# Kernel tuning notes

Hardware: AMD Instinct MI355X
Metric: run time of the kernel (lower is better)

Reference implementation:

```python
import jax, jax.numpy as jnp
import numpy as np

N = 100000
E = 3200000
F_IN = 256
F_OUT = 256
HID = 64


def setup_inputs() -> dict:
    key = jax.random.key(0)
    ks = jax.random.split(key, 16)
    stdv = 1.0 / np.sqrt(F_OUT)
    std_att = 1.0 / np.sqrt(HID)
    std_att_vec = 1.0 / np.sqrt(3.0)
    u = lambda k, shape, s: jax.random.uniform(k, shape, jnp.float32, -s, s)
    return {
        "inputx": jax.random.normal(ks[0], (N, F_IN), jnp.float32),
        "row_A": jax.random.randint(ks[1], (E,), 0, N),
        "col_A": jax.random.randint(ks[2], (E,), 0, N),
        "val_A": jax.random.uniform(ks[3], (E,), jnp.float32),
        "row_A2": jax.random.randint(ks[4], (E,), 0, N),
        "col_A2": jax.random.randint(ks[5], (E,), 0, N),
        "val_A2": jax.random.uniform(ks[6], (E,), jnp.float32),
        "weight_A": u(ks[7], (F_IN, F_OUT), stdv),
        "weight_A2": u(ks[8], (F_IN, F_OUT), stdv),
        "weight_mlp": u(ks[9], (F_IN, F_OUT), stdv),
        "W_k0": u(ks[10], (F_OUT, HID), std_att),
        "W_k1": u(ks[11], (F_OUT, HID), std_att),
        "W_k2": u(ks[12], (F_OUT, HID), std_att),
        "att_vec_A": u(ks[13], (F_OUT, HID), std_att),
        "att_vec_A2": u(ks[14], (F_OUT, HID), std_att),
        "att_vec_mlp": u(ks[15], (F_OUT, HID), std_att),
        "att_vec": u(jax.random.fold_in(key, 99), (3, 3), std_att_vec),
    }


def _spmm(row, col, val, x, n):
    # COO sparse-dense matmul: out[r] += val_e * x[c]
    return jax.ops.segment_sum(val[:, None] * x[col], row, num_segments=n)


def reference(inputx, row_A, col_A, val_A, row_A2, col_A2, val_A2,
              weight_A, weight_A2, weight_mlp, W_k0, W_k1, W_k2,
              att_vec_A, att_vec_A2, att_vec_mlp, att_vec):
    n = inputx.shape[0]
    out_A = jax.nn.relu(_spmm(row_A, col_A, val_A, inputx @ weight_A, n))
    out_A2 = jax.nn.relu(_spmm(row_A2, col_A2, val_A2, inputx @ weight_A2, n))
    out_mlp = jax.nn.relu(inputx @ weight_mlp)
    # attention gating
    T = 3.0
    k0 = jnp.mean(out_A @ W_k0, axis=0, keepdims=True)    # [1, HID]
    k1 = jnp.mean(out_A2 @ W_k1, axis=0, keepdims=True)
    k2 = jnp.mean(out_mlp @ W_k2, axis=0, keepdims=True)
    logits = jnp.concatenate([
        (out_A @ att_vec_A) @ k0.T,      # [N, 1]
        (out_A2 @ att_vec_A2) @ k1.T,
        (out_mlp @ att_vec_mlp) @ k2.T,
    ], axis=1)                           # [N, 3]
    att = jax.nn.softmax((jax.nn.sigmoid(logits) @ att_vec) / T, axis=1)
    return 3.0 * (att[:, 0:1] * out_A + att[:, 1:2] * out_A2 + att[:, 2:3] * out_mlp)
```

## Files before the change

kernel.cpp:

```cpp
#include <hip/hip_runtime.h>

typedef __bf16 bf16;
typedef __bf16 bf16x4 __attribute__((ext_vector_type(4)));
typedef __bf16 bf16x8 __attribute__((ext_vector_type(8)));
typedef float f32x4 __attribute__((ext_vector_type(4)));

__device__ __forceinline__ f32x4 bf2f(bf16x4 v){
  f32x4 r; r[0]=(float)v[0]; r[1]=(float)v[1]; r[2]=(float)v[2]; r[3]=(float)v[3]; return r;
}

#define NBMAX 1600
#define NBP   1601
#define CHUNK 4096
#define CAP   2560
#define CSRCAP 2816

__global__ __launch_bounds__(256) void k_xcvt(const float* __restrict__ X, bf16* __restrict__ Xb, int total){
  int i = (blockIdx.x*256 + threadIdx.x)*8;
  if (i + 8 <= total){
    float4 a = *(const float4*)(X+i);
    float4 b = *(const float4*)(X+i+4);
    bf16x8 v;
    v[0]=(bf16)a.x; v[1]=(bf16)a.y; v[2]=(bf16)a.z; v[3]=(bf16)a.w;
    v[4]=(bf16)b.x; v[5]=(bf16)b.y; v[6]=(bf16)b.z; v[7]=(bf16)b.w;
    *(bf16x8*)(Xb+i) = v;
  }
}

__global__ __launch_bounds__(256) void k_wt(const float* __restrict__ W0, const float* __restrict__ W1,
                                            const float* __restrict__ W2, bf16* __restrict__ WT3){
  int n = blockIdx.x, mat = blockIdx.y, k = threadIdx.x;
  const float* W = (mat==0)?W0:((mat==1)?W1:W2);
  WT3[mat*65536 + n*256 + k] = (bf16)W[k*256 + n];
}

__global__ __launch_bounds__(512) void k_binT(const int* __restrict__ rowA, const int* __restrict__ colA,
    const float* __restrict__ valA, const int* __restrict__ rowA2, const int* __restrict__ colA2,
    const float* __restrict__ valA2, int* __restrict__ gcur,
    int2* __restrict__ pTA, int2* __restrict__ pTA2, int E, int NB){
  __shared__ int hist[NBMAX];
  int mat = blockIdx.y;
  const int* row = mat? rowA2 : rowA;
  const int* col = mat? colA2 : colA;
  const float* val = mat? valA2 : valA;
  int2* pT = mat? pTA2 : pTA;
  int t = threadIdx.x;
  for (int i=t; i<NB; i+=512) hist[i] = 0;
  __syncthreads();
  int base = blockIdx.x * CHUNK;
  int endi = base + CHUNK; if (endi > E) endi = E;
  for (int i = base + t; i < endi; i += 512) atomicAdd(&hist[row[i] >> 6], 1);
  __syncthreads();
  for (int i=t; i<NB; i+=512){
    int c = hist[i];
    if (c) hist[i] = i*CAP + atomicAdd(&gcur[mat*NB + i], c);
  }
  __syncthreads();
  for (int i = base + t; i < endi; i += 512){
    int r = row[i];
    int pos = atomicAdd(&hist[r >> 6], 1);
    int2 p; p.x = ((r & 63) << 17) | col[i]; p.y = __float_as_int(val[i]);
    pT[pos] = p;
  }
}

__global__ __launch_bounds__(256) void k_bscan(const int* __restrict__ gcur, int* __restrict__ gstart,
    int NB, int E){
  __shared__ int ss[256];
  __shared__ int carry;
  int mat = blockIdx.x;
  int t = threadIdx.x;
  if (t==0) carry = 0;
  __syncthreads();
  for (int base=0; base<NB; base+=256){
    int i = base + t;
    int v = (i < NB) ? gcur[mat*NB + i] : 0;
    ss[t] = v; __syncthreads();
    for (int off=1; off<256; off<<=1){
      int u = (t>=off)? ss[t-off] : 0;
      __syncthreads();
      ss[t] += u;
      __syncthreads();
    }
    int excl = carry + ss[t] - v;
    if (i < NB) gstart[mat*NBP + i] = excl;
    int tot = ss[255];
    __syncthreads();
    if (t==0) carry += tot;
    __syncthreads();
  }
  if (t==0) gstart[mat*NBP + NB] = E;
}

__global__ __launch_bounds__(256) void k_csr(const int2* __restrict__ pTA, const int2* __restrict__ pTA2,
    const int* __restrict__ gcur, const int* __restrict__ gstart,
    int* __restrict__ rsA, int* __restrict__ rsA2,
    int2* __restrict__ permA, int2* __restrict__ permA2, int N, int NB, int E){
  __shared__ int2 raw[CSRCAP];
  __shared__ unsigned short sidx[CSRCAP];
  __shared__ int fill[64];
  __shared__ int rowst_l[64];
  int mat = blockIdx.y;
  const int2* pT = mat? pTA2 : pTA;
  int2* perm = mat? permA2 : permA;
  int* rs = mat? rsA2 : rsA;
  int b = blockIdx.x;
  int t = threadIdx.x;
  int r0 = b*64;
  int src = b*CAP;
  int cnt = gcur[mat*NB + b];
  if (cnt > CSRCAP) cnt = CSRCAP;
  int dst = gstart[mat*NBP + b];
  if (t < 64) fill[t] = 0;
  __syncthreads();
  for (int i = t; i < cnt; i += 256){
    int2 e = pT[src + i];
    raw[i] = e;
    atomicAdd(&fill[e.x >> 17], 1);
  }
  __syncthreads();
  if (t < 64){
    int v = fill[t];
    int x = v;
#pragma unroll
    for (int off=1; off<64; off<<=1){
      int u = __shfl_up(x, off, 64);
      if (t >= off) x += u;
    }
    int st = x - v;
    rowst_l[t] = st;
    if (r0 + t < N) rs[r0 + t] = dst + st;
    fill[t] = 0;
  }
  __syncthreads();
  for (int i = t; i < cnt; i += 256){
    int rl = raw[i].x >> 17;
    int pos = atomicAdd(&fill[rl], 1);
    sidx[rowst_l[rl] + pos] = (unsigned short)i;
  }
  __syncthreads();
  for (int j = t; j < cnt; j += 256){
    int2 e = raw[sidx[j]];
    int2 o; o.x = e.x & 0x1FFFF; o.y = e.y;
    perm[dst + j] = o;
  }
  if (t == 0 && b == NB-1) rs[N] = E;
}

__global__ __launch_bounds__(256) void k_spmm(const bf16* __restrict__ Xb,
    const int* __restrict__ rsA, const int* __restrict__ rsA2,
    const int2* __restrict__ permA, const int2* __restrict__ permA2,
    bf16* __restrict__ AXb, bf16* __restrict__ A2Xb, int N){
  int mat = blockIdx.y;
  const int* rs = mat? rsA2 : rsA;
  const int2* perm = mat? permA2 : permA;
  bf16* dst = mat? A2Xb : AXb;
  int t = threadIdx.x, lane = t & 63, wv = t >> 6;
  int c = lane*4;
  int rstep = gridDim.x*4;

  for (int row = blockIdx.x*4 + wv; row < N; row += rstep){
    int e = rs[row], eend = rs[row+1];
    f32x4 acc; acc[0]=0.f; acc[1]=0.f; acc[2]=0.f; acc[3]=0.f;

    int2 p0, p1, p2, p3;
    bool have = (e + 3 < eend);
    if (have){ p0 = perm[e]; p1 = perm[e+1]; p2 = perm[e+2]; p3 = perm[e+3]; }
    while (have){
      bf16x4 g0 = *(const bf16x4*)(Xb + (size_t)p0.x*256 + c);
      bf16x4 g1 = *(const bf16x4*)(Xb + (size_t)p1.x*256 + c);
      bf16x4 g2 = *(const bf16x4*)(Xb + (size_t)p2.x*256 + c);
      bf16x4 g3 = *(const bf16x4*)(Xb + (size_t)p3.x*256 + c);
      float v0 = __int_as_float(p0.y), v1 = __int_as_float(p1.y);
      float v2 = __int_as_float(p2.y), v3 = __int_as_float(p3.y);
      e += 4;
      have = (e + 3 < eend);
      if (have){ p0 = perm[e]; p1 = perm[e+1]; p2 = perm[e+2]; p3 = perm[e+3]; }
      acc += v0 * bf2f(g0);
      acc += v1 * bf2f(g1);
      acc += v2 * bf2f(g2);
      acc += v3 * bf2f(g3);
    }
    for (; e < eend; ++e){
      int2 p = perm[e];
      acc += __int_as_float(p.y) * bf2f(*(const bf16x4*)(Xb + (size_t)p.x*256 + c));
    }
    bf16x4 o;
#pragma unroll
    for (int k=0;k<4;k++) o[k] = (bf16)acc[k];
    *(bf16x4*)(dst + (size_t)row*256 + c) = o;
  }
}

__global__ __launch_bounds__(512) void k_gemm(bf16* __restrict__ M0, bf16* __restrict__ M1,
        bf16* __restrict__ M2, const bf16* __restrict__ WT3, float* __restrict__ colsum, int N){
  __shared__ __align__(16) bf16 sA[128*32];
  __shared__ __align__(16) bf16 sB[256*32];
  __shared__ float gcs[256];
  int t = threadIdx.x;
  int lane = t & 63, wave = t>>6, wm = wave>>2, wn = wave&3;
  int mat = blockIdx.y;
  int m0 = blockIdx.x*128;
  const bf16* WT = WT3 + mat*65536;
  bf16* M = (mat==0)?M0:((mat==1)?M1:M2);

  f32x4 acc[4][4];
#pragma unroll
  for (int i=0;i<4;i++)
#pragma unroll
    for (int j=0;j<4;j++){ acc[i][j][0]=0.f; acc[i][j][1]=0.f; acc[i][j][2]=0.f; acc[i][j][3]=0.f; }

  int ar = t>>2, ac = t&3;
  int alc = ac ^ ((ar>>1)&3);
  int agrow = m0 + ar; if (agrow > N-1) agrow = N-1;
  const bf16* gA = M + (size_t)agrow*256 + alc*8;
  bf16* lA = sA + ar*32 + ac*8;

  int br = t>>2, bc = t&3;
  int blc = bc ^ ((br>>1)&3);
  const bf16* gB0 = WT + br*256 + blc*8;
  const bf16* gB1 = WT + (br+128)*256 + blc*8;
  bf16* lB0 = sB + br*32 + bc*8;
  bf16* lB1 = sB + (br+128)*32 + bc*8;

  for (int k0=0; k0<256; k0+=32){
    __syncthreads();
    *(bf16x8*)lA  = *(const bf16x8*)(gA  + k0);
    *(bf16x8*)lB0 = *(const bf16x8*)(gB0 + k0);
    *(bf16x8*)lB1 = *(const bf16x8*)(gB1 + k0);
    __syncthreads();

    bf16x8 af[4], bfr[4];
#pragma unroll
    for (int i=0;i<4;i++){
      int arow = wm*64 + i*16 + (lane&15);
      int pc = (lane>>4) ^ ((arow>>1)&3);
      af[i] = *(const bf16x8*)(sA + arow*32 + pc*8);
    }
#pragma unroll
    for (int j=0;j<4;j++){
      int brow = wn*64 + j*16 + (lane&15);
      int pc = (lane>>4) ^ ((brow>>1)&3);
      bfr[j] = *(const bf16x8*)(sB + brow*32 + pc*8);
    }
#pragma unroll
    for (int i=0;i<4;i++)
#pragma unroll
      for (int j=0;j<4;j++)
        acc[i][j] = __builtin_amdgcn_mfma_f32_16x16x32_bf16(af[i], bfr[j], acc[i][j], 0,0,0);
  }

  int col0 = wn*64 + (lane&15);
  int rb = m0 + wm*64 + ((lane>>4)<<2);
  float pj[4] = {0.f,0.f,0.f,0.f};
#pragma unroll
  for (int i=0;i<4;i++){
#pragma unroll
    for (int tt=0; tt<4; tt++){
      int r = rb + i*16 + tt;
      if (r < N){
#pragma unroll
        for (int j=0;j<4;j++){
          float vv = acc[i][j][tt];
          if (vv < 0.f) vv = 0.f;
          pj[j] += vv;
          M[(size_t)r*256 + col0 + j*16] = (bf16)vv;
        }
      }
    }
  }
  if (t < 256) gcs[t] = 0.f;
  __syncthreads();
#pragma unroll
  for (int j=0;j<4;j++) atomicAdd(&gcs[col0 + j*16], pj[j]);
  __syncthreads();
  if (t < 256) atomicAdd(&colsum[mat*256 + t], gcs[t]);
}

__global__ void k_attn(const float* __restrict__ colsum,
    const float* __restrict__ Wk0, const float* __restrict__ Wk1, const float* __restrict__ Wk2,
    const float* __restrict__ V0, const float* __restrict__ V1, const float* __restrict__ V2,
    float* __restrict__ wvec, int N){
  __shared__ float smean[768];
  __shared__ float sk[192];
  int t = threadIdx.x;
  float invN = 1.f/(float)N;
  smean[t]     = colsum[t]     * invN;
  smean[t+256] = colsum[t+256] * invN;
  smean[t+512] = colsum[t+512] * invN;
  __syncthreads();
  if (t < 192){
    int j = t>>6, h = t&63;
    const float* Wk = (j==0)?Wk0:((j==1)?Wk1:Wk2);
    float s = 0.f;
    for (int cc=0; cc<256; cc++) s += smean[j*256+cc]*Wk[cc*64+h];
    sk[j*64+h] = s;
  }
  __syncthreads();
  int c = t;
  for (int j=0;j<3;j++){
    const float* V = (j==0)?V0:((j==1)?V1:V2);
    float s = 0.f;
    for (int h=0;h<64;h++) s += V[c*64+h]*sk[j*64+h];
    wvec[j*256+c] = s;
  }
}

__global__ __launch_bounds__(256) void k_epi(const bf16* __restrict__ A, const bf16* __restrict__ B,
    const bf16* __restrict__ M, const float* __restrict__ wvec, const float* __restrict__ av9,
    float* __restrict__ out, int N){
  __shared__ float sw[768];
  __shared__ float sav[9];
  int t = threadIdx.x;
  sw[t] = wvec[t]; sw[t+256] = wvec[t+256]; sw[t+512] = wvec[t+512];
  if (t < 9) sav[t] = av9[t];
  __syncthreads();
  int row = blockIdx.x*4 + (t>>6);
  if (row >= N) return;
  int lane = t & 63;
  int c = lane*4;
  f32x4 a = bf2f(*(const bf16x4*)(A + (size_t)row*256 + c));
  f32x4 b = bf2f(*(const bf16x4*)(B + (size_t)row*256 + c));
  f32x4 m = bf2f(*(const bf16x4*)(M + (size_t)row*256 + c));
  float p0 = a[0]*sw[c] + a[1]*sw[c+1] + a[2]*sw[c+2] + a[3]*sw[c+3];
  float p1 = b[0]*sw[256+c] + b[1]*sw[256+c+1] + b[2]*sw[256+c+2] + b[3]*sw[256+c+3];
  float p2 = m[0]*sw[512+c] + m[1]*sw[512+c+1] + m[2]*sw[512+c+2] + m[3]*sw[512+c+3];
#pragma unroll
  for (int off=32; off>=1; off>>=1){
    p0 += __shfl_xor(p0, off);
    p1 += __shfl_xor(p1, off);
    p2 += __shfl_xor(p2, off);
  }
  float s0 = 1.f/(1.f+expf(-p0));
  float s1 = 1.f/(1.f+expf(-p1));
  float s2 = 1.f/(1.f+expf(-p2));
  float g0 = (s0*sav[0] + s1*sav[3] + s2*sav[6]) * (1.f/3.f);
  float g1 = (s0*sav[1] + s1*sav[4] + s2*sav[7]) * (1.f/3.f);
  float g2 = (s0*sav[2] + s1*sav[5] + s2*sav[8]) * (1.f/3.f);
  float mx = fmaxf(g0, fmaxf(g1,g2));
  float e0 = expf(g0-mx), e1 = expf(g1-mx), e2 = expf(g2-mx);
  float inv = 3.f/(e0+e1+e2);
  float a0 = e0*inv, a1 = e1*inv, a2 = e2*inv;
  f32x4 o = a0*a + a1*b + a2*m;
  *(f32x4*)(out + (size_t)row*256 + c) = o;
}

extern "C" void kernel_launch(void* const* d_in, const int* in_sizes, int n_in,
                              void* d_out, int out_size, void* d_ws, size_t ws_size,
                              hipStream_t stream){
  const float* X    = (const float*)d_in[0];
  const int*   rowA = (const int*)d_in[1];
  const int*   colA = (const int*)d_in[2];
  const float* valA = (const float*)d_in[3];
  const int*   rowA2= (const int*)d_in[4];
  const int*   colA2= (const int*)d_in[5];
  const float* valA2= (const float*)d_in[6];
  const float* W0   = (const float*)d_in[7];
  const float* W1   = (const float*)d_in[8];
  const float* W2   = (const float*)d_in[9];
  const float* Wk0  = (const float*)d_in[10];
  const float* Wk1  = (const float*)d_in[11];
  const float* Wk2  = (const float*)d_in[12];
  const float* V0   = (const float*)d_in[13];
  const float* V1   = (const float*)d_in[14];
  const float* V2   = (const float*)d_in[15];
  const float* AV9  = (const float*)d_in[16];
  int N = in_sizes[0] / 256;
  int E = in_sizes[1];
  int NB = (N + 63) >> 6;
  int ebl2 = (E + CHUNK-1)/CHUNK;

  char* ws = (char*)d_ws;
  size_t off = 0;
  auto take = [&](size_t b)->char*{ char* r = ws + off; off = (off + b + 255) & ~(size_t)255; return r; };
  size_t mb = (size_t)N*256*2;
  bf16* WT3  = (bf16*)take((size_t)3*256*256*2);
  bf16* Xb   = (bf16*)take(mb);
  bf16* B1   = (bf16*)take(mb);
  bf16* B2   = (bf16*)take(mb);
  int* rsA    = (int*)take((size_t)(N+1)*4);
  int* rsA2   = (int*)take((size_t)(N+1)*4);
  int* gcur   = (int*)take((size_t)2*NB*4);
  int* gstart = (int*)take((size_t)2*NBP*4);
  float* colsum = (float*)take(768*4);
  float* wvec   = (float*)take(768*4);
  int2* permA  = (int2*)take((size_t)E*8);
  int2* permA2 = (int2*)take((size_t)E*8);
  int2* pTA  = (int2*)B1;
  int2* pTA2 = (int2*)B2;

  hipMemsetAsync(gcur, 0, (size_t)2*NB*4, stream);
  hipMemsetAsync(colsum, 0, 768*4, stream);

  int total = N*256;
  k_xcvt<<<dim3((total/8 + 255)/256),256,0,stream>>>(X, Xb, total);
  k_wt<<<dim3(256,3),256,0,stream>>>(W0,W1,W2,WT3);
  k_binT<<<dim3(ebl2,2),512,0,stream>>>(rowA,colA,valA,rowA2,colA2,valA2,gcur,pTA,pTA2,E,NB);
  k_bscan<<<2,256,0,stream>>>(gcur,gstart,NB,E);
  k_csr<<<dim3(NB,2),256,0,stream>>>(pTA,pTA2,gcur,gstart,rsA,rsA2,permA,permA2,N,NB,E);
  int sblk = (N+31)/32;
  k_spmm<<<dim3(sblk,2),256,0,stream>>>(Xb,rsA,rsA2,permA,permA2,B1,B2,N);
  k_gemm<<<dim3((N+127)/128,3),512,0,stream>>>(B1,B2,Xb,WT3,colsum,N);
  k_attn<<<1,256,0,stream>>>(colsum,Wk0,Wk1,Wk2,V0,V1,V2,wvec,N);
  k_epi<<<dim3((N+3)/4),256,0,stream>>>(B1,B2,Xb,wvec,AV9,(float*)d_out,N);
}
```

Before: 1.028 ms.

## Coarsen COO binning to 256-row buckets with locally sorted coalesced scatter

Row buckets grow from 64 to 256 rows and edge chunks from 4096 to 8192. The binning kernel now does a local counting sort in shared memory, so each bucket's edges are written to the staging buffer as contiguous runs instead of scattered single writes. The CSR kernel re-reads staged entries from global memory rather than caching them in shared memory, so each block can cover 256 rows with 512 threads. The aim is fewer global atomics and better-coalesced scatter writes, at the cost of extra shared-memory scan passes and repeated global reads in the CSR step.

```diff
diff --git a/kernel.cpp b/kernel.cpp
--- a/kernel.cpp
+++ b/kernel.cpp
@@ -9,11 +9,11 @@
   f32x4 r; r[0]=(float)v[0]; r[1]=(float)v[1]; r[2]=(float)v[2]; r[3]=(float)v[3]; return r;
 }
 
-#define NBMAX 1600
-#define NBP   1601
-#define CHUNK 4096
-#define CAP   2560
-#define CSRCAP 2816
+#define RB    256
+#define NBMAX 400
+#define NBP   401
+#define CHUNK 8192
+#define CAP   9216
 
 __global__ __launch_bounds__(256) void k_xcvt(const float* __restrict__ X, bf16* __restrict__ Xb, int total){
   int i = (blockIdx.x*256 + threadIdx.x)*8;
@@ -39,6 +39,11 @@
     const float* __restrict__ valA2, int* __restrict__ gcur,
     int2* __restrict__ pTA, int2* __restrict__ pTA2, int E, int NB){
   __shared__ int hist[NBMAX];
+  __shared__ int lstart[NBMAX];
+  __shared__ int delta[NBMAX];
+  __shared__ int ss[512];
+  __shared__ unsigned short sidx[CHUNK];
+  __shared__ unsigned short bop[CHUNK];
   int mat = blockIdx.y;
   const int* row = mat? rowA2 : rowA;
   const int* col = mat? colA2 : colA;
@@ -49,18 +54,39 @@
   __syncthreads();
   int base = blockIdx.x * CHUNK;
   int endi = base + CHUNK; if (endi > E) endi = E;
-  for (int i = base + t; i < endi; i += 512) atomicAdd(&hist[row[i] >> 6], 1);
-  __syncthreads();
-  for (int i=t; i<NB; i+=512){
-    int c = hist[i];
-    if (c) hist[i] = i*CAP + atomicAdd(&gcur[mat*NB + i], c);
+  int cnt = endi - base;
+  for (int i = base + t; i < endi; i += 512) atomicAdd(&hist[row[i] >> 8], 1);
+  __syncthreads();
+  int v = (t < NB) ? hist[t] : 0;
+  ss[t] = v; __syncthreads();
+  for (int off=1; off<512; off<<=1){
+    int u = (t>=off)? ss[t-off] : 0;
+    __syncthreads();
+    ss[t] += u;
+    __syncthreads();
+  }
+  if (t < NB){
+    int excl = ss[t] - v;
+    lstart[t] = excl;
+    int ofs = v ? atomicAdd(&gcur[mat*NB + t], v) : 0;
+    if (ofs > CAP - v) ofs = (CAP - v > 0) ? CAP - v : 0;
+    delta[t] = (t*CAP + ofs) - excl;
+    hist[t] = 0;
   }
   __syncthreads();
   for (int i = base + t; i < endi; i += 512){
+    int b = row[i] >> 8;
+    int lpos = lstart[b] + atomicAdd(&hist[b], 1);
+    sidx[lpos] = (unsigned short)(i - base);
+    bop[lpos]  = (unsigned short)b;
+  }
+  __syncthreads();
+  for (int j = t; j < cnt; j += 512){
+    int i = base + (int)sidx[j];
+    int b = bop[j];
     int r = row[i];
-    int pos = atomicAdd(&hist[r >> 6], 1);
-    int2 p; p.x = ((r & 63) << 17) | col[i]; p.y = __float_as_int(val[i]);
-    pT[pos] = p;
+    int2 p; p.x = ((r & 255) << 17) | col[i]; p.y = __float_as_int(val[i]);
+    pT[delta[b] + j] = p;
   }
 }
 
@@ -92,55 +118,52 @@
   if (t==0) gstart[mat*NBP + NB] = E;
 }
 
-__global__ __launch_bounds__(256) void k_csr(const int2* __restrict__ pTA, const int2* __restrict__ pTA2,
+__global__ __launch_bounds__(512) void k_csr(const int2* __restrict__ pTA, const int2* __restrict__ pTA2,
     const int* __restrict__ gcur, const int* __restrict__ gstart,
     int* __restrict__ rsA, int* __restrict__ rsA2,
     int2* __restrict__ permA, int2* __restrict__ permA2, int N, int NB, int E){
-  __shared__ int2 raw[CSRCAP];
-  __shared__ unsigned short sidx[CSRCAP];
-  __shared__ int fill[64];
-  __shared__ int rowst_l[64];
+  __shared__ unsigned short sidx[CAP];
+  __shared__ int fill[RB];
+  __shared__ int rowst[RB];
+  __shared__ int ss[512];
   int mat = blockIdx.y;
   const int2* pT = mat? pTA2 : pTA;
   int2* perm = mat? permA2 : permA;
   int* rs = mat? rsA2 : rsA;
   int b = blockIdx.x;
   int t = threadIdx.x;
-  int r0 = b*64;
+  int r0 = b*RB;
   int src = b*CAP;
   int cnt = gcur[mat*NB + b];
-  if (cnt > CSRCAP) cnt = CSRCAP;
+  if (cnt > CAP) cnt = CAP;
   int dst = gstart[mat*NBP + b];
-  if (t < 64) fill[t] = 0;
-  __syncthreads();
-  for (int i = t; i < cnt; i += 256){
-    int2 e = pT[src + i];
-    raw[i] = e;
-    atomicAdd(&fill[e.x >> 17], 1);
-  }
-  __syncthreads();
-  if (t < 64){
-    int v = fill[t];
-    int x = v;
-#pragma unroll
-    for (int off=1; off<64; off<<=1){
-      int u = __shfl_up(x, off, 64);
-      if (t >= off) x += u;
-    }
-    int st = x - v;
-    rowst_l[t] = st;
-    if (r0 + t < N) rs[r0 + t] = dst + st;
+  if (t < RB) fill[t] = 0;
+  __syncthreads();
+  for (int i = t; i < cnt; i += 512) atomicAdd(&fill[pT[src + i].x >> 17], 1);
+  __syncthreads();
+  int v = (t < RB) ? fill[t] : 0;
+  ss[t] = v; __syncthreads();
+  for (int off=1; off<512; off<<=1){
+    int u = (t>=off)? ss[t-off] : 0;
+    __syncthreads();
+    ss[t] += u;
+    __syncthreads();
+  }
+  if (t < RB){
+    int excl = ss[t] - v;
+    rowst[t] = excl;
+    if (r0 + t < N) rs[r0 + t] = dst + excl;
     fill[t] = 0;
   }
   __syncthreads();
-  for (int i = t; i < cnt; i += 256){
-    int rl = raw[i].x >> 17;
-    int pos = atomicAdd(&fill[rl], 1);
-    sidx[rowst_l[rl] + pos] = (unsigned short)i;
-  }
-  __syncthreads();
-  for (int j = t; j < cnt; j += 256){
-    int2 e = raw[sidx[j]];
+  for (int i = t; i < cnt; i += 512){
+    int rl = pT[src + i].x >> 17;
+    int lp = rowst[rl] + atomicAdd(&fill[rl], 1);
+    sidx[lp] = (unsigned short)i;
+  }
+  __syncthreads();
+  for (int j = t; j < cnt; j += 512){
+    int2 e = pT[src + (int)sidx[j]];
     int2 o; o.x = e.x & 0x1FFFF; o.y = e.y;
     perm[dst + j] = o;
   }
@@ -367,8 +390,8 @@
   const float* AV9  = (const float*)d_in[16];
   int N = in_sizes[0] / 256;
   int E = in_sizes[1];
-  int NB = (N + 63) >> 6;
-  int ebl2 = (E + CHUNK-1)/CHUNK;
+  int NB = (N + RB-1) >> 8;
+  int ebl = (E + CHUNK-1)/CHUNK;
 
   char* ws = (char*)d_ws;
   size_t off = 0;
@@ -395,9 +418,9 @@
   int total = N*256;
   k_xcvt<<<dim3((total/8 + 255)/256),256,0,stream>>>(X, Xb, total);
   k_wt<<<dim3(256,3),256,0,stream>>>(W0,W1,W2,WT3);
-  k_binT<<<dim3(ebl2,2),512,0,stream>>>(rowA,colA,valA,rowA2,colA2,valA2,gcur,pTA,pTA2,E,NB);
+  k_binT<<<dim3(ebl,2),512,0,stream>>>(rowA,colA,valA,rowA2,colA2,valA2,gcur,pTA,pTA2,E,NB);
   k_bscan<<<2,256,0,stream>>>(gcur,gstart,NB,E);
-  k_csr<<<dim3(NB,2),256,0,stream>>>(pTA,pTA2,gcur,gstart,rsA,rsA2,permA,permA2,N,NB,E);
+  k_csr<<<dim3(NB,2),512,0,stream>>>(pTA,pTA2,gcur,gstart,rsA,rsA2,permA,permA2,N,NB,E);
   int sblk = (N+31)/32;
   k_spmm<<<dim3(sblk,2),256,0,stream>>>(Xb,rsA,rsA2,permA,permA2,B1,B2,N);
   k_gemm<<<dim3((N+127)/128,3),512,0,stream>>>(B1,B2,Xb,WT3,colsum,N);
```

Result: no change. 1.019 ms (-0.8%).
